# Kernel tuning notes

Hardware: AMD Instinct MI355X
Metric: run time of the kernel (lower is better)

## Reference

```python
import jax, jax.numpy as jnp
import numpy as np

N = 50000   # nodes
IN = 256    # in_dim == hidden_dim
HID = 256
H = 4       # heads
HD = 64     # head_dim = HID // H
L = 2       # layers
E = 20000   # hyperedges
M = 320000  # incidence pairs
TQ = 64     # type_query_dim


def setup_inputs() -> dict:
    key = jax.random.key(0)
    ks = jax.random.split(key, 12)
    s = 0.05
    return {
        "x": jax.random.normal(ks[0], (N, IN), jnp.float32),
        "node_types": jax.random.randint(ks[1], (N,), 0, 3),
        "edge_type": jax.random.randint(ks[2], (E,), 0, 3),
        "node_idx": jax.random.randint(ks[3], (M,), 0, N),
        "edge_idx": jax.random.randint(ks[4], (M,), 0, E),
        # stacked per-layer, per-head parameters
        "tq": jax.random.normal(ks[5], (L, H, 3, TQ), jnp.float32) * s,      # type_query embedding
        "w1": jax.random.normal(ks[6], (L, H, 32, IN + TQ), jnp.float32) * s,  # type_attention_fc[0]
        "b1": jnp.zeros((L, H, 32), jnp.float32),
        "w2": jax.random.normal(ks[7], (L, H, 32), jnp.float32) * s,          # type_attention_fc[2]
        "b2": jnp.zeros((L, H), jnp.float32),
        "wq": jax.random.normal(ks[8], (L, H, HD, IN), jnp.float32) * s,      # query (no bias)
        "wv": jax.random.normal(ks[9], (L, H, HD, IN), jnp.float32) * s,      # value (no bias)
        "ec": jax.random.normal(ks[10], (L, H, 3, HD), jnp.float32) * s,      # edge_context embedding
        "ln_g": jnp.ones((L, HID), jnp.float32),
        "ln_b": jnp.zeros((L, HID), jnp.float32),
    }


def reference(x, node_types, edge_type, node_idx, edge_idx,
              tq, w1, b1, w2, b2, wq, wv, ec, ln_g, ln_b):
    h = x
    et_pair = edge_type[edge_idx]  # [M] edge type per incidence pair
    for l in range(L):
        # --- per-node type gate (alpha_type) ---
        sigs = jnp.moveaxis(tq[l], 0, 1)[node_types]                     # [N,H,TQ]
        hid = jnp.tanh(jnp.einsum('nd,hkd->nhk', h, w1[l, :, :, :IN])
                       + jnp.einsum('nhd,hkd->nhk', sigs, w1[l, :, :, IN:])
                       + b1[l][None])                                    # [N,H,32]
        alpha_type = jax.nn.sigmoid(jnp.einsum('nhk,hk->nh', hid, w2[l]) + b2[l][None])  # [N,H]
        # --- Q/V projections ---
        Q = jnp.einsum('nd,hod->nho', h, wq[l])                          # [N,H,HD]
        V = jnp.einsum('nd,hod->nho', h, wv[l])                          # [N,H,HD]
        ctx = jnp.moveaxis(ec[l], 0, 1)[et_pair]                         # [M,H,HD]
        # --- per-incidence attention logits ---
        alpha = jax.nn.leaky_relu(jnp.einsum('mho,mho->mh', Q[node_idx], ctx), 0.2)
        alpha = alpha * alpha_type[node_idx]                             # [M,H]
        # --- segment softmax over edges ---
        mx = jax.ops.segment_max(alpha, edge_idx, num_segments=E)        # [E,H]
        ex = jnp.exp(alpha - mx[edge_idx])
        den = jax.ops.segment_sum(ex, edge_idx, num_segments=E)
        attn = ex / den[edge_idx]                                        # [M,H]
        # --- dual scatter-add: node->edge then edge->node ---
        edge_feat = jax.ops.segment_sum(attn[:, :, None] * V[node_idx], edge_idx, num_segments=E)   # [E,H,HD]
        node_feat = jax.ops.segment_sum(attn[:, :, None] * edge_feat[edge_idx], node_idx, num_segments=N)  # [N,H,HD]
        # skip (identity since in_dim==hidden) + residual + LayerNorm
        h = h + node_feat.reshape(N, HID)
        mu = jnp.mean(h, -1, keepdims=True)
        var = jnp.mean((h - mu) ** 2, -1, keepdims=True)
        h = (h - mu) * jax.lax.rsqrt(var + 1e-5) * ln_g[l] + ln_b[l]
    return h
```

## Files before the change

### kernel.cpp

```cpp
#include <hip/hip_runtime.h>
#include <hip/hip_bf16.h>

typedef __hip_bfloat16 bf16;
using short8  = __attribute__((ext_vector_type(8))) short;
using float4v = __attribute__((ext_vector_type(4))) float;

static constexpr int N_ = 50000;
static constexpr int E_ = 20000;
static constexpr int M_ = 320000;
static constexpr int NPAD_ = 50048;
static constexpr int NB_E = (E_+255)/256;
static constexpr int NB_N = (N_+255)/256;

__device__ __forceinline__ float b2f(bf16 v){ return __bfloat162float(v); }
__device__ __forceinline__ float sigm(float x){ return 1.f/(1.f+__expf(-x)); }
__device__ __forceinline__ float u2f(unsigned short u){ return __uint_as_float(((unsigned)u)<<16); }
__device__ __forceinline__ unsigned short f2u(float f){ bf16 t=__float2bfloat16(f); return *(unsigned short*)&t; }

__global__ __launch_bounds__(256) void k_sniff(const unsigned short* __restrict__ xb, int* flag){
  int tid = threadIdx.x;
  int sane = 0;
  for (int i = tid; i < 4096; i += 256){
    unsigned short u = xb[2*i];
    int ex = (u >> 7) & 0xFF;
    if ((u & 0x7FFF) == 0 || (ex >= 117 && ex <= 137)) sane++;
  }
  #pragma unroll
  for (int d=1; d<64; d<<=1) sane += __shfl_xor(sane, d, 64);
  __shared__ int wsh[4];
  if ((tid&63)==0) wsh[tid>>6] = sane;
  __syncthreads();
  if (tid==0){
    int tot = wsh[0]+wsh[1]+wsh[2]+wsh[3];
    *flag = (tot > 2048) ? 1 : 0;
  }
}

__global__ __launch_bounds__(256) void k_cvt16(const void* __restrict__ src, bf16* __restrict__ dst,
                                               int n, const int* __restrict__ flag){
  int i = blockIdx.x*256 + threadIdx.x;
  if (i >= n) return;
  if (*flag) dst[i] = ((const bf16*)src)[i];
  else       dst[i] = __float2bfloat16(((const float*)src)[i]);
}

__global__ __launch_bounds__(256) void k_cvtall(
    const void* s0, const void* s1, const void* s2, const void* s3, const void* s4,
    const void* s5, const void* s6, const void* s7, const void* s8, const void* s9,
    float* d0, float* d1, float* d2, float* d3, float* d4,
    float* d5, float* d6, float* d7, float* d8, float* d9,
    const int* __restrict__ flag){
  int i = blockIdx.x*256 + threadIdx.x;
  const void* src; float* dst; int off;
  if      (i < 1536)            { src=s0; dst=d0; off=i; }
  else if (i < 1536+81920)      { src=s1; dst=d1; off=i-1536; }
  else if (i < 83712+256)       { src=s2; dst=d2; off=i-83712; }
  else if (i < 83968+256)       { src=s3; dst=d3; off=i-83968; }
  else if (i < 84224+8)         { src=s4; dst=d4; off=i-84224; }
  else if (i < 84232+131072)    { src=s5; dst=d5; off=i-84232; }
  else if (i < 215304+131072)   { src=s6; dst=d6; off=i-215304; }
  else if (i < 346376+1536)     { src=s7; dst=d7; off=i-346376; }
  else if (i < 347912+512)      { src=s8; dst=d8; off=i-347912; }
  else if (i < 348424+512)      { src=s9; dst=d9; off=i-348424; }
  else return;
  if (*flag) dst[off] = b2f(((const bf16*)src)[off]);
  else       dst[off] = ((const float*)src)[off];
}

__global__ __launch_bounds__(256) void k_zero2(int* pe, int* pn){
  int i = blockIdx.x*256 + threadIdx.x;
  if (i < E_) pe[i] = 0;
  else if (i < E_+N_) pn[i-E_] = 0;
}

__global__ __launch_bounds__(256) void k_hist(const int* __restrict__ eidx, const int* __restrict__ nidx,
                                              int* cnt_e, int* cnt_n){
  int m = blockIdx.x*256 + threadIdx.x;
  if (m < M_){ atomicAdd(&cnt_e[eidx[m]],1); atomicAdd(&cnt_n[nidx[m]],1); }
}

__device__ __forceinline__ void scan1_body(const int* cnt, int* off, int* bsum, int n, int blk){
  int tid = threadIdx.x, lane = tid&63, wid = tid>>6;
  int i = blk*256 + tid;
  int v = (i<n)? cnt[i] : 0;
  int s = v;
  #pragma unroll
  for (int d=1; d<64; d<<=1){ int t = __shfl_up(s, d, 64); if (lane>=d) s += t; }
  __shared__ int ws[4]; __shared__ int wo[4];
  if (lane==63) ws[wid] = s;
  __syncthreads();
  if (tid==0){ int a=0; for (int k=0;k<4;k++){ int t=ws[k]; wo[k]=a; a+=t; } bsum[blk]=a; }
  __syncthreads();
  if (i<n) off[i] = wo[wid] + s - v;
}

__global__ __launch_bounds__(256) void k_scan1m(const int* __restrict__ cnt_e, int* __restrict__ eoff, int* bsum_e,
                                                const int* __restrict__ cnt_n, int* __restrict__ noff, int* bsum_n){
  int b = blockIdx.x;
  if (b < NB_E) scan1_body(cnt_e, eoff, bsum_e, E_, b);
  else          scan1_body(cnt_n, noff, bsum_n, N_, b-NB_E);
}

__device__ __forceinline__ void scan2_body(int* bsum, int* off, int nb, int n){
  int tid = threadIdx.x, lane = tid&63, wid = tid>>6;
  int v = (tid<nb)? bsum[tid] : 0;
  int s = v;
  #pragma unroll
  for (int d=1; d<64; d<<=1){ int t = __shfl_up(s, d, 64); if (lane>=d) s += t; }
  __shared__ int ws[4]; __shared__ int wo[4];
  if (lane==63) ws[wid] = s;
  __syncthreads();
  if (tid==0){ int a=0; for (int k=0;k<4;k++){ int t=ws[k]; wo[k]=a; a+=t; } off[n]=a; }
  __syncthreads();
  if (tid<nb) bsum[tid] = wo[wid] + s - v;
}

__global__ __launch_bounds__(256) void k_scan2m(int* bsum_e, int* __restrict__ eoff,
                                                int* bsum_n, int* __restrict__ noff){
  if (blockIdx.x == 0) scan2_body(bsum_e, eoff, NB_E, E_);
  else                 scan2_body(bsum_n, noff, NB_N, N_);
}

__global__ __launch_bounds__(256) void k_scan3m(const int* __restrict__ bsum_e, int* __restrict__ eoff, int* cur_e,
                                                const int* __restrict__ bsum_n, int* __restrict__ noff, int* cur_n){
  int b = blockIdx.x;
  if (b < NB_E){
    int i = b*256 + threadIdx.x;
    if (i<E_){ int e = eoff[i] + bsum_e[b]; eoff[i]=e; cur_e[i]=e; }
  } else {
    int i = (b-NB_E)*256 + threadIdx.x;
    if (i<N_){ int e = noff[i] + bsum_n[b-NB_E]; noff[i]=e; cur_n[i]=e; }
  }
}

__global__ __launch_bounds__(256) void k_fill(const int* __restrict__ eidx, const int* __restrict__ nidx,
                                              int* cur_e, int* cur_n, int* ep, int* np){
  int m = blockIdx.x*256 + threadIdx.x;
  if (m < M_){
    int p = atomicAdd(&cur_e[eidx[m]],1); ep[p]=m;
    int q = atomicAdd(&cur_n[nidx[m]],1); np[q]=m;
  }
}

__global__ __launch_bounds__(256) void k_pre(const float* __restrict__ tq, const float* __restrict__ w1,
                                             const float* __restrict__ b1, float* __restrict__ pre){
  int idx = blockIdx.x*256 + threadIdx.x;
  if (idx >= 768) return;
  int l = idx / 384, r = idx % 384;
  int t = r / 128, r2 = r % 128;
  int h = r2 >> 5, k = r2 & 31;
  const float* tp = tq + ((l*4+h)*3 + t)*64;
  const float* wp = w1 + (size_t)((l*4+h)*32 + k)*320 + 256;
  float s = b1[(l*4+h)*32 + k];
  for (int d=0; d<64; ++d) s += tp[d]*wp[d];
  pre[(l*3+t)*128 + r2] = s;
}

__global__ __launch_bounds__(256) void k_wqe(const float* __restrict__ wq_f, const float* __restrict__ ec_f,
                                             float* __restrict__ wqe){
  int b = blockIdx.x;
  int l = b/12, ht = b%12, h = ht/3, t = ht%3;
  int d = threadIdx.x;
  const float* ecp = ec_f + ((l*4+h)*3 + t)*64;
  const float* wqp = wq_f + (size_t)((l*4+h)*64)*256;
  float s = 0.f;
  for (int o=0;o<64;++o) s += ecp[o]*wqp[o*256 + d];
  wqe[(size_t)(l*12+ht)*256 + d] = s;
}

__global__ __launch_bounds__(256) void k_bpack(const float* __restrict__ wv_f, const float* __restrict__ w1_f,
                                               const float* __restrict__ wqe, bf16* __restrict__ Bp){
  int idx = blockIdx.x*256 + threadIdx.x;
  if (idx >= 2*448*256) return;
  int l = idx / (448*256), r = idx % (448*256);
  int c = r >> 8, k = r & 255;
  float v = 0.f;
  if (c < 256){
    int dd = c >> 2, h = c & 3;
    v = wv_f[(size_t)l*65536 + (size_t)(h*64+dd)*256 + k];
  }
  else if (c < 384) v = w1_f[(size_t)l*40960 + (size_t)(c-256)*320 + k];
  else if (c < 396) v = wqe[(size_t)(l*12 + c-384)*256 + k];
  Bp[idx] = __float2bfloat16(v);
}

__global__ __launch_bounds__(256,3) void k_mgemm(const bf16* __restrict__ A16, const bf16* __restrict__ Bp,
    bf16* __restrict__ V16, bf16* __restrict__ Hb16, float* __restrict__ S){
  int g = blockIdx.x;
  int xcd = g & 7, i7 = g >> 3;
  int wgid = (xcd==0) ? i7 : (343 + (xcd-1)*342 + i7);
  int x = wgid % 7, y = wgid / 7;

  int t = threadIdx.x;
  int wid = t >> 6, lane = t & 63;
  int q = lane >> 4, li = lane & 15;
  int row0blk = y*128;
  int col0 = x*64;
  int w32 = wid*32;

  __shared__ char lds[49152];

  float4v acc[2][4];
  #pragma unroll
  for (int i=0;i<2;i++)
    #pragma unroll
    for (int j=0;j<4;j++) acc[i][j] = (float4v)(0.f);

  auto stage = [&](int st, int buf){
    const int k0 = st*64;
    char* lA = lds + (buf ? 24576 : 0);
    char* lB = lds + (buf ? 40960 : 16384);
    const bf16* Asrc = A16 + (size_t)row0blk*256 + k0;
    const bf16* Bsrc = Bp  + (size_t)col0*256 + k0;
    #pragma unroll
    for (int ra=0; ra<4; ++ra){
      int gidx = ra*256 + t;
      int r = gidx >> 3, c = gidx & 7;
      const bf16* src = Asrc + (size_t)r*256 + ((c ^ (r&7)) << 3);
      char* dst = lA + (ra*256 + wid*64)*16;
      __builtin_amdgcn_global_load_lds((const __attribute__((address_space(1))) void*)src,
                                       (__attribute__((address_space(3))) void*)dst, 16, 0, 0);
    }
    #pragma unroll
    for (int rb=0; rb<2; ++rb){
      int gidx = rb*256 + t;
      int r = gidx >> 3, c = gidx & 7;
      const bf16* src = Bsrc + (size_t)r*256 + ((c ^ (r&7)) << 3);
      char* dst = lB + (rb*256 + wid*64)*16;
      __builtin_amdgcn_global_load_lds((const __attribute__((address_space(1))) void*)src,
                                       (__attribute__((address_space(3))) void*)dst, 16, 0, 0);
    }
  };

  stage(0, 0);
  #pragma unroll
  for (int st=0; st<4; ++st){
    int bufc = st & 1;
    if (st < 3) stage(st+1, bufc^1);
    __builtin_amdgcn_sched_barrier(0);
    if (st < 3) asm volatile("s_waitcnt vmcnt(6)" ::: "memory");
    else        asm volatile("s_waitcnt vmcnt(0)" ::: "memory");
    __builtin_amdgcn_s_barrier();
    __builtin_amdgcn_sched_barrier(0);

    const char* cA = lds + (bufc ? 24576 : 0);
    const char* cB = lds + (bufc ? 40960 : 16384);
    short8 af[2][2], bfr[4][2];
    #pragma unroll
    for (int i=0;i<2;i++)
      #pragma unroll
      for (int k2=0;k2<2;k2++){
        int row = w32 + i*16 + li;
        int gr = (k2*4 + q) ^ (li & 7);
        af[i][k2] = *(const short8*)(cA + row*128 + gr*16);
      }
    #pragma unroll
    for (int j=0;j<4;j++)
      #pragma unroll
      for (int k2=0;k2<2;k2++){
        int row = j*16 + li;
        int gr = (k2*4 + q) ^ (li & 7);
        bfr[j][k2] = *(const short8*)(cB + row*128 + gr*16);
      }
    #pragma unroll
    for (int k2=0;k2<2;k2++)
      #pragma unroll
      for (int j=0;j<4;j++){
        acc[0][j] = __builtin_amdgcn_mfma_f32_16x16x32_bf16(af[0][k2], bfr[j][k2], acc[0][j],0,0,0);
        acc[1][j] = __builtin_amdgcn_mfma_f32_16x16x32_bf16(af[1][k2], bfr[j][k2], acc[1][j],0,0,0);
      }
    __builtin_amdgcn_sched_barrier(0);
    __builtin_amdgcn_s_barrier();
  }

  int row0 = row0blk + w32;
  #pragma unroll
  for (int i=0;i<2;i++){
    #pragma unroll
    for (int r=0;r<4;r++){
      int grow = row0 + i*16 + q*4 + r;
      if (grow >= N_) continue;
      #pragma unroll
      for (int j=0;j<4;j++){
        int gc = col0 + j*16 + li;
        float v = acc[i][j][r];
        if (gc < 256)      V16 [(size_t)grow*256 + gc]       = __float2bfloat16(v);
        else if (gc < 384) Hb16[(size_t)grow*128 + gc - 256] = __float2bfloat16(v);
        else if (gc < 396) S   [(size_t)grow*12  + gc - 384] = v;
      }
    }
  }
}

__global__ __launch_bounds__(256) void k_gate(const unsigned short* __restrict__ Hb16, const float* __restrict__ S,
    const float* __restrict__ pre_l, const float* __restrict__ w2_l, const float* __restrict__ b2_l,
    const int* __restrict__ ntype, float* __restrict__ G){
  int node = blockIdx.x*4 + (threadIdx.x>>6);
  int lane = threadIdx.x & 63;
  if (node >= N_) return;
  int typ = ntype[node];
  const float* pr = pre_l + typ*128;
  float v0 = tanhf(u2f(Hb16[(size_t)node*128 + lane])      + pr[lane]);
  float v1 = tanhf(u2f(Hb16[(size_t)node*128 + 64 + lane]) + pr[64+lane]);
  float p0 = v0 * w2_l[lane];
  float p1 = v1 * w2_l[64+lane];
  #pragma unroll
  for (int d=1; d<32; d<<=1){ p0 += __shfl_xor(p0,d,64); p1 += __shfl_xor(p1,d,64); }
  float at0 = sigm(__shfl(p0, 0,64) + b2_l[0]);
  float at1 = sigm(__shfl(p0,32,64) + b2_l[1]);
  float at2 = sigm(__shfl(p1, 0,64) + b2_l[2]);
  float at3 = sigm(__shfl(p1,32,64) + b2_l[3]);
  if (lane < 12){
    int h = lane / 3, t = lane % 3;
    float sv = S[(size_t)node*12 + lane];
    float lr = (sv > 0.f) ? sv : 0.2f*sv;
    float av = (h==0)? at0 : (h==1)? at1 : (h==2)? at2 : at3;
    G[(size_t)node*12 + t*4 + h] = lr * av;
  }
}

__global__ __launch_bounds__(256) void k_edge(const int* __restrict__ eoff, const int* __restrict__ ep,
    const int* __restrict__ nidx, const int* __restrict__ etype,
    const float* __restrict__ G, const unsigned short* __restrict__ V16,
    float* __restrict__ attn, unsigned short* __restrict__ EF16){
  int e = blockIdx.x*4 + (threadIdx.x>>6);
  int lane = threadIdx.x & 63;
  if (e >= E_) return;
  int beg = eoff[e], end = eoff[e+1];
  int deg = end - beg;
  if (deg == 0) return;
  int t = etype[e];
  float a0=0,a1=0,a2=0,a3=0;

  if (deg <= 64){
    int i = beg + lane;
    int m = -1, n = 0;
    float4 g; g.x=g.y=g.z=g.w=-1e30f;
    if (lane < deg){
      m = ep[i]; n = nidx[m];
      g = *(const float4*)(G + (size_t)n*12 + t*4);
    }
    float mx0=g.x, mx1=g.y, mx2=g.z, mx3=g.w;
    #pragma unroll
    for (int d=1; d<64; d<<=1){
      mx0=fmaxf(mx0,__shfl_xor(mx0,d,64)); mx1=fmaxf(mx1,__shfl_xor(mx1,d,64));
      mx2=fmaxf(mx2,__shfl_xor(mx2,d,64)); mx3=fmaxf(mx3,__shfl_xor(mx3,d,64));
    }
    float ex0=0,ex1=0,ex2=0,ex3=0;
    if (lane < deg){
      ex0=__expf(g.x-mx0); ex1=__expf(g.y-mx1); ex2=__expf(g.z-mx2); ex3=__expf(g.w-mx3);
    }
    float s0=ex0,s1=ex1,s2=ex2,s3=ex3;
    #pragma unroll
    for (int d=1; d<64; d<<=1){
      s0+=__shfl_xor(s0,d,64); s1+=__shfl_xor(s1,d,64);
      s2+=__shfl_xor(s2,d,64); s3+=__shfl_xor(s3,d,64);
    }
    float4 w; w.x=ex0/s0; w.y=ex1/s1; w.z=ex2/s2; w.w=ex3/s3;
    if (lane < deg) *(float4*)(attn + (size_t)m*4) = w;
    auto ldrow = [&](int j)->ushort4{
      int nn = __shfl(n, j, 64);
      return *(const ushort4*)(V16 + (size_t)nn*256 + (lane<<2));
    };
    ushort4 v0v,v1v,v2v,v3v;
    if (deg>0) v0v=ldrow(0);
    if (deg>1) v1v=ldrow(1);
    if (deg>2) v2v=ldrow(2);
    if (deg>3) v3v=ldrow(3);
    for (int j=0;j<deg;j+=4){
      { float wx=__shfl(w.x,j,64),wy=__shfl(w.y,j,64),wz=__shfl(w.z,j,64),wq=__shfl(w.w,j,64);
        a0+=wx*u2f(v0v.x); a1+=wy*u2f(v0v.y); a2+=wz*u2f(v0v.z); a3+=wq*u2f(v0v.w);
        if (j+4<deg) v0v=ldrow(j+4); }
      if (j+1<deg){
        float wx=__shfl(w.x,j+1,64),wy=__shfl(w.y,j+1,64),wz=__shfl(w.z,j+1,64),wq=__shfl(w.w,j+1,64);
        a0+=wx*u2f(v1v.x); a1+=wy*u2f(v1v.y); a2+=wz*u2f(v1v.z); a3+=wq*u2f(v1v.w);
        if (j+5<deg) v1v=ldrow(j+5); }
      if (j+2<deg){
        float wx=__shfl(w.x,j+2,64),wy=__shfl(w.y,j+2,64),wz=__shfl(w.z,j+2,64),wq=__shfl(w.w,j+2,64);
        a0+=wx*u2f(v2v.x); a1+=wy*u2f(v2v.y); a2+=wz*u2f(v2v.z); a3+=wq*u2f(v2v.w);
        if (j+6<deg) v2v=ldrow(j+6); }
      if (j+3<deg){
        float wx=__shfl(w.x,j+3,64),wy=__shfl(w.y,j+3,64),wz=__shfl(w.z,j+3,64),wq=__shfl(w.w,j+3,64);
        a0+=wx*u2f(v3v.x); a1+=wy*u2f(v3v.y); a2+=wz*u2f(v3v.z); a3+=wq*u2f(v3v.w);
        if (j+7<deg) v3v=ldrow(j+7); }
    }
  } else {
    float mx0=-1e30f, mx1=-1e30f, mx2=-1e30f, mx3=-1e30f;
    for (int i=beg+lane; i<end; i+=64){
      int m = ep[i]; int n = nidx[m];
      float4 g = *(const float4*)(G + (size_t)n*12 + t*4);
      mx0=fmaxf(mx0,g.x); mx1=fmaxf(mx1,g.y); mx2=fmaxf(mx2,g.z); mx3=fmaxf(mx3,g.w);
    }
    #pragma unroll
    for (int d=1; d<64; d<<=1){
      mx0=fmaxf(mx0,__shfl_xor(mx0,d,64)); mx1=fmaxf(mx1,__shfl_xor(mx1,d,64));
      mx2=fmaxf(mx2,__shfl_xor(mx2,d,64)); mx3=fmaxf(mx3,__shfl_xor(mx3,d,64));
    }
    float sm0=0,sm1=0,sm2=0,sm3=0;
    for (int i=beg+lane; i<end; i+=64){
      int m = ep[i]; int n = nidx[m];
      float4 g = *(const float4*)(G + (size_t)n*12 + t*4);
      sm0+=__expf(g.x-mx0); sm1+=__expf(g.y-mx1); sm2+=__expf(g.z-mx2); sm3+=__expf(g.w-mx3);
    }
    #pragma unroll
    for (int d=1; d<64; d<<=1){
      sm0+=__shfl_xor(sm0,d,64); sm1+=__shfl_xor(sm1,d,64);
      sm2+=__shfl_xor(sm2,d,64); sm3+=__shfl_xor(sm3,d,64);
    }
    float inv0=1.f/sm0, inv1=1.f/sm1, inv2=1.f/sm2, inv3=1.f/sm3;
    for (int i=beg+lane; i<end; i+=64){
      int m = ep[i]; int n = nidx[m];
      float4 g = *(const float4*)(G + (size_t)n*12 + t*4);
      float4 w;
      w.x=__expf(g.x-mx0)*inv0; w.y=__expf(g.y-mx1)*inv1;
      w.z=__expf(g.z-mx2)*inv2; w.w=__expf(g.w-mx3)*inv3;
      *(float4*)(attn + (size_t)m*4) = w;
    }
    for (int i=beg; i<end; ++i){
      int m = ep[i]; int n = nidx[m];
      float4 g = *(const float4*)(G + (size_t)n*12 + t*4);
      float w0=__expf(g.x-mx0)*inv0, w1=__expf(g.y-mx1)*inv1;
      float w2=__expf(g.z-mx2)*inv2, w3=__expf(g.w-mx3)*inv3;
      ushort4 v = *(const ushort4*)(V16 + (size_t)n*256 + lane*4);
      a0 += w0*u2f(v.x); a1 += w1*u2f(v.y); a2 += w2*u2f(v.z); a3 += w3*u2f(v.w);
    }
  }
  ushort4 ev; ev.x=f2u(a0); ev.y=f2u(a1); ev.z=f2u(a2); ev.w=f2u(a3);
  *(ushort4*)(EF16 + (size_t)e*256 + lane*4) = ev;
}

__global__ __launch_bounds__(256) void k_node(const int* __restrict__ noff, const int* __restrict__ np,
    const int* __restrict__ eidx, const float* __restrict__ attn, const unsigned short* __restrict__ EF16,
    const float* __restrict__ lng, const float* __restrict__ lnb,
    bf16* __restrict__ h16, void* __restrict__ outv, const int* __restrict__ flag, int last){
  int n = blockIdx.x*4 + (threadIdx.x>>6);
  int lane = threadIdx.x & 63;
  if (n >= N_) return;
  float f0=0,f1=0,f2=0,f3=0;
  int beg = noff[n], end = noff[n+1];
  int deg = end - beg;
  if (deg > 0 && deg <= 64){
    int i = beg + lane;
    int e = 0;
    float4 w; w.x=w.y=w.z=w.w=0.f;
    if (lane < deg){
      int m = np[i]; e = eidx[m];
      w = *(const float4*)(attn + (size_t)m*4);
    }
    auto ldrow = [&](int j)->ushort4{
      int ee = __shfl(e, j, 64);
      return *(const ushort4*)(EF16 + (size_t)ee*256 + (lane<<2));
    };
    ushort4 v0v,v1v,v2v,v3v;
    if (deg>0) v0v=ldrow(0);
    if (deg>1) v1v=ldrow(1);
    if (deg>2) v2v=ldrow(2);
    if (deg>3) v3v=ldrow(3);
    for (int j=0;j<deg;j+=4){
      { float wx=__shfl(w.x,j,64),wy=__shfl(w.y,j,64),wz=__shfl(w.z,j,64),wq=__shfl(w.w,j,64);
        f0+=wx*u2f(v0v.x); f1+=wy*u2f(v0v.y); f2+=wz*u2f(v0v.z); f3+=wq*u2f(v0v.w);
        if (j+4<deg) v0v=ldrow(j+4); }
      if (j+1<deg){
        float wx=__shfl(w.x,j+1,64),wy=__shfl(w.y,j+1,64),wz=__shfl(w.z,j+1,64),wq=__shfl(w.w,j+1,64);
        f0+=wx*u2f(v1v.x); f1+=wy*u2f(v1v.y); f2+=wz*u2f(v1v.z); f3+=wq*u2f(v1v.w);
        if (j+5<deg) v1v=ldrow(j+5); }
      if (j+2<deg){
        float wx=__shfl(w.x,j+2,64),wy=__shfl(w.y,j+2,64),wz=__shfl(w.z,j+2,64),wq=__shfl(w.w,j+2,64);
        f0+=wx*u2f(v2v.x); f1+=wy*u2f(v2v.y); f2+=wz*u2f(v2v.z); f3+=wq*u2f(v2v.w);
        if (j+6<deg) v2v=ldrow(j+6); }
      if (j+3<deg){
        float wx=__shfl(w.x,j+3,64),wy=__shfl(w.y,j+3,64),wz=__shfl(w.z,j+3,64),wq=__shfl(w.w,j+3,64);
        f0+=wx*u2f(v3v.x); f1+=wy*u2f(v3v.y); f2+=wz*u2f(v3v.z); f3+=wq*u2f(v3v.w);
        if (j+7<deg) v3v=ldrow(j+7); }
    }
  } else if (deg > 64){
    for (int i=beg; i<end; ++i){
      int m = np[i]; int e = eidx[m];
      float4 w = *(const float4*)(attn + (size_t)m*4);
      ushort4 v = *(const ushort4*)(EF16 + (size_t)e*256 + lane*4);
      f0 += w.x*u2f(v.x); f1 += w.y*u2f(v.y); f2 += w.z*u2f(v.z); f3 += w.w*u2f(v.w);
    }
  }
  const bf16* hp = h16 + (size_t)n*256;
  float h0 = b2f(hp[lane])+f0, h1 = b2f(hp[64+lane])+f1, h2 = b2f(hp[128+lane])+f2, h3 = b2f(hp[192+lane])+f3;
  float s = h0+h1+h2+h3;
  #pragma unroll
  for (int d=1; d<64; d<<=1) s += __shfl_xor(s,d,64);
  float mean = s * (1.f/256.f);
  float d0=h0-mean, d1=h1-mean, d2=h2-mean, d3=h3-mean;
  float vv = d0*d0+d1*d1+d2*d2+d3*d3;
  #pragma unroll
  for (int d=1; d<64; d<<=1) vv += __shfl_xor(vv,d,64);
  float rstd = rsqrtf(vv*(1.f/256.f) + 1e-5f);
  float o0 = d0*rstd*lng[lane]     + lnb[lane];
  float o1 = d1*rstd*lng[64+lane]  + lnb[64+lane];
  float o2 = d2*rstd*lng[128+lane] + lnb[128+lane];
  float o3 = d3*rstd*lng[192+lane] + lnb[192+lane];
  if (last){
    if (*flag){
      bf16* op = (bf16*)outv + (size_t)n*256;
      op[lane]=__float2bfloat16(o0); op[64+lane]=__float2bfloat16(o1);
      op[128+lane]=__float2bfloat16(o2); op[192+lane]=__float2bfloat16(o3);
    } else {
      float* op = (float*)outv + (size_t)n*256;
      op[lane]=o0; op[64+lane]=o1; op[128+lane]=o2; op[192+lane]=o3;
    }
  } else {
    bf16* o16 = h16 + (size_t)n*256;
    o16[lane]=__float2bfloat16(o0); o16[64+lane]=__float2bfloat16(o1);
    o16[128+lane]=__float2bfloat16(o2); o16[192+lane]=__float2bfloat16(o3);
  }
}

extern "C" void kernel_launch(void* const* d_in, const int* in_sizes, int n_in,
                              void* d_out, int out_size, void* d_ws, size_t ws_size,
                              hipStream_t stream){
  const void* x    = d_in[0];
  const int* ntype = (const int*)d_in[1];
  const int* etype = (const int*)d_in[2];
  const int* nidx  = (const int*)d_in[3];
  const int* eidx  = (const int*)d_in[4];
  (void)in_sizes; (void)n_in; (void)out_size; (void)ws_size;

  char* ws = (char*)d_ws;
  size_t o = 0;
  auto alloc = [&](size_t b)->char*{ char* r = ws + o; o = (o + b + 255) & ~(size_t)255; return r; };
  int*   flag = (int*)  alloc(256);
  char*  R2   =         alloc((size_t)20000000);
  float* G    = (float*)alloc((size_t)N_*12*4);
  float* tq_f  = (float*)alloc(1536*4);
  float* w1_f  = (float*)alloc(81920*4);
  float* b1_f  = (float*)alloc(256*4);
  float* w2_f  = (float*)alloc(256*4);
  float* b2_f  = (float*)alloc(8*4);
  float* wq_f  = (float*)alloc(131072*4);
  float* wv_f  = (float*)alloc(131072*4);
  float* ec_f  = (float*)alloc(1536*4);
  float* lng_f = (float*)alloc(512*4);
  float* lnb_f = (float*)alloc(512*4);
  float* wqe   = (float*)alloc(6144*4);
  float* pre   = (float*)alloc(768*4);
  int* cnt_e  = (int*)alloc((size_t)E_*4);
  int* cnt_n  = (int*)alloc((size_t)N_*4);
  int* eoff   = (int*)alloc((size_t)(E_+1)*4);
  int* noff   = (int*)alloc((size_t)(N_+1)*4);
  int* cur_e  = (int*)alloc((size_t)E_*4);
  int* cur_n  = (int*)alloc((size_t)N_*4);
  int* ep     = (int*)alloc((size_t)M_*4);
  int* np     = (int*)alloc((size_t)M_*4);
  int* bsum_e = (int*)alloc(256*4);
  int* bsum_n = (int*)alloc(256*4);
  bf16* h16   = (bf16*)alloc((size_t)NPAD_*256*2);
  bf16* Bp    = (bf16*)alloc((size_t)2*448*256*2);
  bf16* V16   = (bf16*)alloc((size_t)N_*256*2);

  bf16*  Hb16 = (bf16*)R2;
  float* S    = (float*)(R2 + 16777216);
  float* attn = (float*)R2;
  unsigned short* EF16 = (unsigned short*)(R2 + 5242880);

  k_sniff<<<1, 256, 0, stream>>>((const unsigned short*)x, flag);
  k_cvt16<<<(N_*256+255)/256, 256, 0, stream>>>(x, h16, N_*256, flag);
  k_cvtall<<<(348936+255)/256, 256, 0, stream>>>(
      d_in[5], d_in[6], d_in[7], d_in[8], d_in[9],
      d_in[10], d_in[11], d_in[12], d_in[13], d_in[14],
      tq_f, w1_f, b1_f, w2_f, b2_f, wq_f, wv_f, ec_f, lng_f, lnb_f, flag);

  k_zero2<<<(E_+N_+255)/256, 256, 0, stream>>>(cnt_e, cnt_n);
  k_hist<<<M_/256, 256, 0, stream>>>(eidx, nidx, cnt_e, cnt_n);
  k_scan1m<<<NB_E+NB_N, 256, 0, stream>>>(cnt_e, eoff, bsum_e, cnt_n, noff, bsum_n);
  k_scan2m<<<2, 256, 0, stream>>>(bsum_e, eoff, bsum_n, noff);
  k_scan3m<<<NB_E+NB_N, 256, 0, stream>>>(bsum_e, eoff, cur_e, bsum_n, noff, cur_n);
  k_fill<<<M_/256, 256, 0, stream>>>(eidx, nidx, cur_e, cur_n, ep, np);
  k_pre<<<3, 256, 0, stream>>>(tq_f, w1_f, b1_f, pre);
  k_wqe<<<24, 256, 0, stream>>>(wq_f, ec_f, wqe);
  k_bpack<<<(2*448*256+255)/256, 256, 0, stream>>>(wv_f, w1_f, wqe, Bp);

  for (int l=0; l<2; ++l){
    k_mgemm<<<2737, 256, 0, stream>>>(h16, Bp + (size_t)l*448*256, V16, Hb16, S);
    k_gate<<<12500, 256, 0, stream>>>((const unsigned short*)Hb16, S, pre + l*384,
                                      w2_f + l*128, b2_f + l*4, ntype, G);
    k_edge<<<5000, 256, 0, stream>>>(eoff, ep, nidx, etype, G, (const unsigned short*)V16, attn, EF16);
    k_node<<<12500, 256, 0, stream>>>(noff, np, eidx, attn, EF16, lng_f + l*256, lnb_f + l*256,
                                      h16, d_out, flag, l==1);
  }
}
```

Baseline: 470.5 us.

## Merge preprocessing kernels to cut launch count in setup phase

```diff
diff --git a/kernel.cpp b/kernel.cpp
--- a/kernel.cpp
+++ b/kernel.cpp
@@ -17,65 +17,67 @@
 __device__ __forceinline__ float u2f(unsigned short u){ return __uint_as_float(((unsigned)u)<<16); }
 __device__ __forceinline__ unsigned short f2u(float f){ bf16 t=__float2bfloat16(f); return *(unsigned short*)&t; }
 
-__global__ __launch_bounds__(256) void k_sniff(const unsigned short* __restrict__ xb, int* flag){
-  int tid = threadIdx.x;
-  int sane = 0;
-  for (int i = tid; i < 4096; i += 256){
-    unsigned short u = xb[2*i];
-    int ex = (u >> 7) & 0xFF;
-    if ((u & 0x7FFF) == 0 || (ex >= 117 && ex <= 137)) sane++;
-  }
-  #pragma unroll
-  for (int d=1; d<64; d<<=1) sane += __shfl_xor(sane, d, 64);
-  __shared__ int wsh[4];
-  if ((tid&63)==0) wsh[tid>>6] = sane;
-  __syncthreads();
-  if (tid==0){
-    int tot = wsh[0]+wsh[1]+wsh[2]+wsh[3];
-    *flag = (tot > 2048) ? 1 : 0;
-  }
-}
-
-__global__ __launch_bounds__(256) void k_cvt16(const void* __restrict__ src, bf16* __restrict__ dst,
-                                               int n, const int* __restrict__ flag){
-  int i = blockIdx.x*256 + threadIdx.x;
-  if (i >= n) return;
-  if (*flag) dst[i] = ((const bf16*)src)[i];
-  else       dst[i] = __float2bfloat16(((const float*)src)[i]);
-}
-
-__global__ __launch_bounds__(256) void k_cvtall(
+__global__ __launch_bounds__(256) void k_sniffzero(const unsigned short* __restrict__ xb, int* flag,
+                                                   int* cnt_e, int* cnt_n){
+  int b = blockIdx.x, tid = threadIdx.x;
+  if (b == 0){
+    int sane = 0;
+    for (int i = tid; i < 4096; i += 256){
+      unsigned short u = xb[2*i];
+      int ex = (u >> 7) & 0xFF;
+      if ((u & 0x7FFF) == 0 || (ex >= 117 && ex <= 137)) sane++;
+    }
+    #pragma unroll
+    for (int d=1; d<64; d<<=1) sane += __shfl_xor(sane, d, 64);
+    __shared__ int wsh[4];
+    if ((tid&63)==0) wsh[tid>>6] = sane;
+    __syncthreads();
+    if (tid==0){
+      int tot = wsh[0]+wsh[1]+wsh[2]+wsh[3];
+      *flag = (tot > 2048) ? 1 : 0;
+    }
+  } else {
+    int i = (b-1)*256 + tid;
+    if (i < E_) cnt_e[i] = 0;
+    else if (i < E_+N_) cnt_n[i-E_] = 0;
+  }
+}
+
+__global__ __launch_bounds__(256) void k_prep(
+    const void* __restrict__ x, bf16* __restrict__ h16,
     const void* s0, const void* s1, const void* s2, const void* s3, const void* s4,
     const void* s5, const void* s6, const void* s7, const void* s8, const void* s9,
     float* d0, float* d1, float* d2, float* d3, float* d4,
     float* d5, float* d6, float* d7, float* d8, float* d9,
+    const int* __restrict__ eidx, const int* __restrict__ nidx,
+    int* cnt_e, int* cnt_n,
     const int* __restrict__ flag){
-  int i = blockIdx.x*256 + threadIdx.x;
-  const void* src; float* dst; int off;
-  if      (i < 1536)            { src=s0; dst=d0; off=i; }
-  else if (i < 1536+81920)      { src=s1; dst=d1; off=i-1536; }
-  else if (i < 83712+256)       { src=s2; dst=d2; off=i-83712; }
-  else if (i < 83968+256)       { src=s3; dst=d3; off=i-83968; }
-  else if (i < 84224+8)         { src=s4; dst=d4; off=i-84224; }
-  else if (i < 84232+131072)    { src=s5; dst=d5; off=i-84232; }
-  else if (i < 215304+131072)   { src=s6; dst=d6; off=i-215304; }
-  else if (i < 346376+1536)     { src=s7; dst=d7; off=i-346376; }
-  else if (i < 347912+512)      { src=s8; dst=d8; off=i-347912; }
-  else if (i < 348424+512)      { src=s9; dst=d9; off=i-348424; }
-  else return;
-  if (*flag) dst[off] = b2f(((const bf16*)src)[off]);
-  else       dst[off] = ((const float*)src)[off];
-}
-
-__global__ __launch_bounds__(256) void k_zero2(int* pe, int* pn){
-  int i = blockIdx.x*256 + threadIdx.x;
-  if (i < E_) pe[i] = 0;
-  else if (i < E_+N_) pn[i-E_] = 0;
-}
-
-__global__ __launch_bounds__(256) void k_hist(const int* __restrict__ eidx, const int* __restrict__ nidx,
-                                              int* cnt_e, int* cnt_n){
-  int m = blockIdx.x*256 + threadIdx.x;
+  int b = blockIdx.x, t = threadIdx.x;
+  if (b < 50000){
+    int i = b*256 + t;
+    if (*flag) h16[i] = ((const bf16*)x)[i];
+    else       h16[i] = __float2bfloat16(((const float*)x)[i]);
+    return;
+  }
+  if (b < 51364){
+    int i = (b-50000)*256 + t;
+    const void* src; float* dst; int off;
+    if      (i < 1536)            { src=s0; dst=d0; off=i; }
+    else if (i < 1536+81920)      { src=s1; dst=d1; off=i-1536; }
+    else if (i < 83712+256)       { src=s2; dst=d2; off=i-83712; }
+    else if (i < 83968+256)       { src=s3; dst=d3; off=i-83968; }
+    else if (i < 84224+8)         { src=s4; dst=d4; off=i-84224; }
+    else if (i < 84232+131072)    { src=s5; dst=d5; off=i-84232; }
+    else if (i < 215304+131072)   { src=s6; dst=d6; off=i-215304; }
+    else if (i < 346376+1536)     { src=s7; dst=d7; off=i-346376; }
+    else if (i < 347912+512)      { src=s8; dst=d8; off=i-347912; }
+    else if (i < 348424+512)      { src=s9; dst=d9; off=i-348424; }
+    else return;
+    if (*flag) dst[off] = b2f(((const bf16*)src)[off]);
+    else       dst[off] = ((const float*)src)[off];
+    return;
+  }
+  int m = (b-51364)*256 + t;
   if (m < M_){ atomicAdd(&cnt_e[eidx[m]],1); atomicAdd(&cnt_n[nidx[m]],1); }
 }
 
@@ -94,83 +96,31 @@
   if (i<n) off[i] = wo[wid] + s - v;
 }
 
-__global__ __launch_bounds__(256) void k_scan1m(const int* __restrict__ cnt_e, int* __restrict__ eoff, int* bsum_e,
-                                                const int* __restrict__ cnt_n, int* __restrict__ noff, int* bsum_n){
+__global__ __launch_bounds__(256) void k_scan1w(
+    const int* __restrict__ cnt_e, int* __restrict__ eoff, int* bsum_e,
+    const int* __restrict__ cnt_n, int* __restrict__ noff, int* bsum_n,
+    const float* __restrict__ tq_f, const float* __restrict__ w1_f, const float* __restrict__ b1_f,
+    float* __restrict__ pre,
+    const float* __restrict__ wv_f, const float* __restrict__ wq_f, const float* __restrict__ ec_f,
+    bf16* __restrict__ Bp){
   int b = blockIdx.x;
-  if (b < NB_E) scan1_body(cnt_e, eoff, bsum_e, E_, b);
-  else          scan1_body(cnt_n, noff, bsum_n, N_, b-NB_E);
-}
-
-__device__ __forceinline__ void scan2_body(int* bsum, int* off, int nb, int n){
-  int tid = threadIdx.x, lane = tid&63, wid = tid>>6;
-  int v = (tid<nb)? bsum[tid] : 0;
-  int s = v;
-  #pragma unroll
-  for (int d=1; d<64; d<<=1){ int t = __shfl_up(s, d, 64); if (lane>=d) s += t; }
-  __shared__ int ws[4]; __shared__ int wo[4];
-  if (lane==63) ws[wid] = s;
-  __syncthreads();
-  if (tid==0){ int a=0; for (int k=0;k<4;k++){ int t=ws[k]; wo[k]=a; a+=t; } off[n]=a; }
-  __syncthreads();
-  if (tid<nb) bsum[tid] = wo[wid] + s - v;
-}
-
-__global__ __launch_bounds__(256) void k_scan2m(int* bsum_e, int* __restrict__ eoff,
-                                                int* bsum_n, int* __restrict__ noff){
-  if (blockIdx.x == 0) scan2_body(bsum_e, eoff, NB_E, E_);
-  else                 scan2_body(bsum_n, noff, NB_N, N_);
-}
-
-__global__ __launch_bounds__(256) void k_scan3m(const int* __restrict__ bsum_e, int* __restrict__ eoff, int* cur_e,
-                                                const int* __restrict__ bsum_n, int* __restrict__ noff, int* cur_n){
-  int b = blockIdx.x;
-  if (b < NB_E){
-    int i = b*256 + threadIdx.x;
-    if (i<E_){ int e = eoff[i] + bsum_e[b]; eoff[i]=e; cur_e[i]=e; }
-  } else {
-    int i = (b-NB_E)*256 + threadIdx.x;
-    if (i<N_){ int e = noff[i] + bsum_n[b-NB_E]; noff[i]=e; cur_n[i]=e; }
-  }
-}
-
-__global__ __launch_bounds__(256) void k_fill(const int* __restrict__ eidx, const int* __restrict__ nidx,
-                                              int* cur_e, int* cur_n, int* ep, int* np){
-  int m = blockIdx.x*256 + threadIdx.x;
-  if (m < M_){
-    int p = atomicAdd(&cur_e[eidx[m]],1); ep[p]=m;
-    int q = atomicAdd(&cur_n[nidx[m]],1); np[q]=m;
-  }
-}
-
-__global__ __launch_bounds__(256) void k_pre(const float* __restrict__ tq, const float* __restrict__ w1,
-                                             const float* __restrict__ b1, float* __restrict__ pre){
-  int idx = blockIdx.x*256 + threadIdx.x;
-  if (idx >= 768) return;
-  int l = idx / 384, r = idx % 384;
-  int t = r / 128, r2 = r % 128;
-  int h = r2 >> 5, k = r2 & 31;
-  const float* tp = tq + ((l*4+h)*3 + t)*64;
-  const float* wp = w1 + (size_t)((l*4+h)*32 + k)*320 + 256;
-  float s = b1[(l*4+h)*32 + k];
-  for (int d=0; d<64; ++d) s += tp[d]*wp[d];
-  pre[(l*3+t)*128 + r2] = s;
-}
-
-__global__ __launch_bounds__(256) void k_wqe(const float* __restrict__ wq_f, const float* __restrict__ ec_f,
-                                             float* __restrict__ wqe){
-  int b = blockIdx.x;
-  int l = b/12, ht = b%12, h = ht/3, t = ht%3;
-  int d = threadIdx.x;
-  const float* ecp = ec_f + ((l*4+h)*3 + t)*64;
-  const float* wqp = wq_f + (size_t)((l*4+h)*64)*256;
-  float s = 0.f;
-  for (int o=0;o<64;++o) s += ecp[o]*wqp[o*256 + d];
-  wqe[(size_t)(l*12+ht)*256 + d] = s;
-}
-
-__global__ __launch_bounds__(256) void k_bpack(const float* __restrict__ wv_f, const float* __restrict__ w1_f,
-                                               const float* __restrict__ wqe, bf16* __restrict__ Bp){
-  int idx = blockIdx.x*256 + threadIdx.x;
+  if (b < NB_E){ scan1_body(cnt_e, eoff, bsum_e, E_, b); return; }
+  if (b < NB_E+NB_N){ scan1_body(cnt_n, noff, bsum_n, N_, b-NB_E); return; }
+  int b2 = b - (NB_E+NB_N);
+  if (b2 < 3){
+    int idx = b2*256 + threadIdx.x;
+    if (idx >= 768) return;
+    int l = idx / 384, r = idx % 384;
+    int t = r / 128, r2 = r % 128;
+    int h = r2 >> 5, k = r2 & 31;
+    const float* tp = tq_f + ((l*4+h)*3 + t)*64;
+    const float* wp = w1_f + (size_t)((l*4+h)*32 + k)*320 + 256;
+    float s = b1_f[(l*4+h)*32 + k];
+    for (int d=0; d<64; ++d) s += tp[d]*wp[d];
+    pre[(l*3+t)*128 + r2] = s;
+    return;
+  }
+  int idx = (b2-3)*256 + threadIdx.x;
   if (idx >= 2*448*256) return;
   int l = idx / (448*256), r = idx % (448*256);
   int c = r >> 8, k = r & 255;
@@ -180,8 +130,43 @@
     v = wv_f[(size_t)l*65536 + (size_t)(h*64+dd)*256 + k];
   }
   else if (c < 384) v = w1_f[(size_t)l*40960 + (size_t)(c-256)*320 + k];
-  else if (c < 396) v = wqe[(size_t)(l*12 + c-384)*256 + k];
+  else if (c < 396){
+    int ht = c-384, h = ht/3, tt = ht%3;
+    const float* ecp = ec_f + ((l*4+h)*3 + tt)*64;
+    const float* wqp = wq_f + (size_t)((l*4+h)*64)*256 + k;
+    float s = 0.f;
+    for (int o2=0; o2<64; ++o2) s += ecp[o2]*wqp[(size_t)o2*256];
+    v = s;
+  }
   Bp[idx] = __float2bfloat16(v);
+}
+
+__global__ __launch_bounds__(256) void k_scan23(const int* __restrict__ bsum_e, int* __restrict__ eoff, int* cur_e,
+                                                const int* __restrict__ bsum_n, int* __restrict__ noff, int* cur_n){
+  int b = blockIdx.x, t = threadIdx.x, lane = t&63, wid = t>>6;
+  int nb, n, blk;
+  const int* bsum; int* off; int* cur;
+  if (b < NB_E){ nb=NB_E; n=E_; bsum=bsum_e; off=eoff; cur=cur_e; blk=b; }
+  else         { nb=NB_N; n=N_; bsum=bsum_n; off=noff; cur=cur_n; blk=b-NB_E; }
+  int v = (t < blk) ? bsum[t] : 0;
+  #pragma unroll
+  for (int d=1; d<64; d<<=1) v += __shfl_xor(v, d, 64);
+  __shared__ int ws[4];
+  if (lane==0) ws[wid] = v;
+  __syncthreads();
+  int p = ws[0]+ws[1]+ws[2]+ws[3];
+  int i = blk*256 + t;
+  if (i < n){ int e = off[i] + p; off[i] = e; cur[i] = e; }
+  if (blk == nb-1 && t == 0) off[n] = p + bsum[nb-1];
+}
+
+__global__ __launch_bounds__(256) void k_fill(const int* __restrict__ eidx, const int* __restrict__ nidx,
+                                              int* cur_e, int* cur_n, int* ep, int* np){
+  int m = blockIdx.x*256 + threadIdx.x;
+  if (m < M_){
+    int p = atomicAdd(&cur_e[eidx[m]],1); ep[p]=m;
+    int q = atomicAdd(&cur_n[nidx[m]],1); np[q]=m;
+  }
 }
 
 __global__ __launch_bounds__(256,3) void k_mgemm(const bf16* __restrict__ A16, const bf16* __restrict__ Bp,
@@ -538,7 +523,6 @@
   float* ec_f  = (float*)alloc(1536*4);
   float* lng_f = (float*)alloc(512*4);
   float* lnb_f = (float*)alloc(512*4);
-  float* wqe   = (float*)alloc(6144*4);
   float* pre   = (float*)alloc(768*4);
   int* cnt_e  = (int*)alloc((size_t)E_*4);
   int* cnt_n  = (int*)alloc((size_t)N_*4);
@@ -559,22 +543,18 @@
   float* attn = (float*)R2;
   unsigned short* EF16 = (unsigned short*)(R2 + 5242880);
 
-  k_sniff<<<1, 256, 0, stream>>>((const unsigned short*)x, flag);
-  k_cvt16<<<(N_*256+255)/256, 256, 0, stream>>>(x, h16, N_*256, flag);
-  k_cvtall<<<(348936+255)/256, 256, 0, stream>>>(
+  k_sniffzero<<<275, 256, 0, stream>>>((const unsigned short*)x, flag, cnt_e, cnt_n);
+  k_prep<<<52614, 256, 0, stream>>>(
+      x, h16,
       d_in[5], d_in[6], d_in[7], d_in[8], d_in[9],
       d_in[10], d_in[11], d_in[12], d_in[13], d_in[14],
-      tq_f, w1_f, b1_f, w2_f, b2_f, wq_f, wv_f, ec_f, lng_f, lnb_f, flag);
-
-  k_zero2<<<(E_+N_+255)/256, 256, 0, stream>>>(cnt_e, cnt_n);
-  k_hist<<<M_/256, 256, 0, stream>>>(eidx, nidx, cnt_e, cnt_n);
-  k_scan1m<<<NB_E+NB_N, 256, 0, stream>>>(cnt_e, eoff, bsum_e, cnt_n, noff, bsum_n);
-  k_scan2m<<<2, 256, 0, stream>>>(bsum_e, eoff, bsum_n, noff);
-  k_scan3m<<<NB_E+NB_N, 256, 0, stream>>>(bsum_e, eoff, cur_e, bsum_n, noff, cur_n);
+      tq_f, w1_f, b1_f, w2_f, b2_f, wq_f, wv_f, ec_f, lng_f, lnb_f,
+      eidx, nidx, cnt_e, cnt_n, flag);
+  k_scan1w<<<NB_E+NB_N+3+896, 256, 0, stream>>>(
+      cnt_e, eoff, bsum_e, cnt_n, noff, bsum_n,
+      tq_f, w1_f, b1_f, pre, wv_f, wq_f, ec_f, Bp);
+  k_scan23<<<NB_E+NB_N, 256, 0, stream>>>(bsum_e, eoff, cur_e, bsum_n, noff, cur_n);
   k_fill<<<M_/256, 256, 0, stream>>>(eidx, nidx, cur_e, cur_n, ep, np);
-  k_pre<<<3, 256, 0, stream>>>(tq_f, w1_f, b1_f, pre);
-  k_wqe<<<24, 256, 0, stream>>>(wq_f, ec_f, wqe);
-  k_bpack<<<(2*448*256+255)/256, 256, 0, stream>>>(wv_f, w1_f, wqe, Bp);
 
   for (int l=0; l<2; ++l){
     k_mgemm<<<2737, 256, 0, stream>>>(h16, Bp + (size_t)l*448*256, V16, Hb16, S);
```

After: 460.0 us. 1.02x faster.
